# Kernel optimization log

Measured on AMD Instinct MI355X. Metric: run time of the kernel, lower is better.

The kernel has to match this reference:

```python
import jax, jax.numpy as jnp
import numpy as np
from jax import lax

CONV_SIZE = 5
MORPH_SIZE = 5
TH1_INIT = 0.5
STEP = 0.0005
LO, HI = 0.84, 0.86


def _maxpool(a):
    p = MORPH_SIZE // 2
    return lax.reduce_window(
        a, -jnp.inf, lax.max,
        window_dimensions=(1, 1, MORPH_SIZE, MORPH_SIZE),
        window_strides=(1, 1, 1, 1),
        padding=[(0, 0), (0, 0), (p, p), (p, p)])


def setup_inputs() -> dict:
    key = jax.random.key(0)
    k1, _ = jax.random.split(key)
    x = jax.random.uniform(k1, (8, 4, 1024, 1024), dtype=jnp.float32)
    blur_k = jnp.full((1, 1, CONV_SIZE, CONV_SIZE), 1.0 / CONV_SIZE ** 2, dtype=jnp.float32)
    return {"x": x, "blur_k": blur_k}


def reference(x, blur_k):
    N, c, h, w = x.shape
    xi = x.reshape(N * c, 1, h, w)
    out = lax.conv_general_dilated(
        xi, blur_k, window_strides=(1, 1), padding='SAME',
        dimension_numbers=('NCHW', 'OIHW', 'NCHW')).reshape(N, c, h, w)

    # iterative mean-based threshold (quantile) search, same as the torch while-loops
    out_c = lax.stop_gradient(out)

    def frac_above(th):
        return jnp.mean(jnp.where(out_c > th, 1.0, 0.0))

    th = jnp.float32(TH1_INIT)
    th = lax.while_loop(lambda t: frac_above(t) < LO, lambda t: t - STEP, th)
    th = lax.while_loop(lambda t: frac_above(t) > HI, lambda t: t + STEP, th)

    thr = jnp.where(out > th, 1.0, 0.0)
    # morphological close: max-pool then min-pool (min = -maxpool(-x))
    closed = -_maxpool(-_maxpool(thr))
    return closed  # torch casts to float64; kept float32 (see notes)
```

## Files before the change

### kernel.cpp

```cpp
#include <hip/hip_runtime.h>


#define K_STEPS 1024
#define LO_COUNT 28185723u
#define R_TILE 16
#define PT_ROWS 16

#define OFF_HIST 4096
#define OFF_KQ   16384

typedef float  fx4 __attribute__((ext_vector_type(4)));

struct TTable { float v[K_STEPS]; };
static constexpr TTable make_T() {
    TTable t{};
    float th = 0.5f;
    for (int k = 0; k < K_STEPS; k++) { t.v[k] = th; th = th - 0.0005f; }
    return t;
}
__device__ constexpr TTable Tc = make_T();

__device__ __forceinline__ uint4 cvt4(float4 f) {
    return make_uint4((unsigned int)(f.x * 8388608.0f),
                      (unsigned int)(f.y * 8388608.0f),
                      (unsigned int)(f.z * 8388608.0f),
                      (unsigned int)(f.w * 8388608.0f));
}

__device__ __forceinline__ int find_ki(const unsigned int* __restrict__ Us,
                                       float gbias, unsigned int s) {
    float g = fmaf(-(float)s, 9.5367432e-6f, gbias);
    int lo = (int)g;
    lo = max(0, min(1022, lo));
    unsigned int a0 = Us[lo], a1 = Us[lo + 1];
    return lo + (int)(s < a0) + (int)(s < a1);
}

__global__ __launch_bounds__(256, 8) void
k_pass1(const float4* __restrict__ x4, const float* __restrict__ bk,
        unsigned int* __restrict__ hist, unsigned short* __restrict__ kq16) {
    __shared__ unsigned int Us[K_STEPS];
    __shared__ unsigned int lh[K_STEPS + 1];
    int tid = threadIdx.x;
    int p = blockIdx.y, y0 = blockIdx.x * R_TILE;
    int wlane = tid & 63;

    {
        double c = (double)bk[0] * (1.0 / 8388608.0);
        #pragma unroll
        for (int i = 0; i < 4; i++) {
            int k = tid + 256 * i;
            double T = (double)Tc.v[k];
            unsigned int u = 0u;
            if (T >= 0.0) {
                u = (unsigned int)(floor(T / c) + 1.0);
                while (u > 0u && (double)(u - 1u) * c > T) u--;
                while (!((double)u * c > T)) u++;
            }
            Us[k] = u;
        }
    }
    for (int i = tid; i < K_STEPS + 1; i += 256) lh[i] = 0u;
    __syncthreads();
    float gbias = fmaf((float)Us[0], 9.5367432e-6f, 0.5f);

    const float4* pf = x4 + (size_t)p * 262144;
    int tB = (tid < 255) ? tid + 1 : 0;
    const uint4 z4 = make_uint4(0u, 0u, 0u, 0u);
    bool edge = (wlane == 63);

    unsigned int cs0 = 0, cs1 = 0, cs2 = 0, cs3 = 0;
    unsigned int cb0 = 0, cb1 = 0, cb2 = 0, cb3 = 0;
    {
        float4 ra[5], rb[5];
        #pragma unroll
        for (int i = 0; i < 5; i++) {
            int yy = y0 - 2 + i, yc = min(max(yy, 0), 1023);
            ra[i] = pf[yc * 256 + tid];
            if (edge) rb[i] = pf[yc * 256 + tB];
        }
        #pragma unroll
        for (int i = 0; i < 5; i++) {
            bool v = (unsigned)(y0 - 2 + i) < 1024u;
            uint4 a = v ? cvt4(ra[i]) : z4;
            cs0 += a.x; cs1 += a.y; cs2 += a.z; cs3 += a.w;
            if (edge) {
                uint4 b = v ? cvt4(rb[i]) : z4;
                cb0 += b.x; cb1 += b.y; cb2 += b.z; cb3 += b.w;
            }
        }
    }
    float4 N0a, N1a, O0a, O1a, NBa, OBa;
    {
        int yn0 = min(y0 + 3, 1023), yn1 = min(y0 + 4, 1023);
        int yo0 = max(y0 - 2, 0),    yo1 = max(y0 - 1, 0);
        N0a = pf[yn0 * 256 + tid]; N1a = pf[yn1 * 256 + tid];
        O0a = pf[yo0 * 256 + tid]; O1a = pf[yo1 * 256 + tid];
        if (edge) { NBa = pf[yn0 * 256 + tB]; OBa = pf[yo0 * 256 + tB]; }
    }

    unsigned int cnt0 = 0;
    #pragma unroll 4
    for (int iy = 0; iy < R_TILE; iy++) {
        int y = y0 + iy;

        unsigned int nc0 = __shfl_down(cs0, 1);
        unsigned int nc1 = __shfl_down(cs1, 1);
        unsigned int nc2 = __shfl_down(cs2, 1);
        unsigned int nc3 = __shfl_down(cs3, 1);
        if (edge) { nc0 = cb0; nc1 = cb1; nc2 = cb2; nc3 = cb3; }

        unsigned int m123 = cs1 + cs2 + cs3;
        unsigned int h45  = nc0 + nc1;
        unsigned int v0, v1, v2, v3;
        if (tid != 255) {
            v0 = cs0 + m123 + nc0;
            v1 = m123 + h45;
            v2 = cs2 + cs3 + h45 + nc2;
            v3 = cs3 + h45 + nc2 + nc3;
        } else {
            v0 = cs0 + m123;
            v1 = m123;
            v2 = h45 + nc2;
            v3 = h45 + nc2 + nc3;
        }

        int k0 = find_ki(Us, gbias, v0);
        int k1 = find_ki(Us, gbias, v1);
        int k2 = find_ki(Us, gbias, v2);
        int k3 = find_ki(Us, gbias, v3);
        cnt0 += (unsigned)(k0 == 0) + (unsigned)(k1 == 0)
              + (unsigned)(k2 == 0) + (unsigned)(k3 == 0);
        if (k0 > 0) atomicAdd(&lh[k0], 1u);
        if (k1 > 0) atomicAdd(&lh[k1], 1u);
        if (k2 > 0) atomicAdd(&lh[k2], 1u);
        if (k3 > 0) atomicAdd(&lh[k3], 1u);

        unsigned int pa = (unsigned)min(k0, 255) | ((unsigned)min(k1, 255) << 8);
        unsigned int pb = (unsigned)min(k2, 255) | ((unsigned)min(k3, 255) << 8);
        unsigned int paN = __shfl_down(pa, 1);
        size_t rb = ((size_t)p * 1024 + (size_t)y) * 512;
        if (wlane < 63) {
            ((unsigned int*)(kq16 + rb))[tid + 1] = pb | (paN << 16);
        } else {
            kq16[rb + ((tid < 255) ? (unsigned)(2 * tid + 2) : 0u)] =
                (unsigned short)pb;
        }
        if (wlane == 0) kq16[rb + 2 * tid + 1] = (unsigned short)pa;

        {
            bool vn = (unsigned)(y + 3) < 1024u;
            bool vo = (y - 2) >= 0;
            uint4 na = vn ? cvt4(N0a) : z4;
            uint4 oa = vo ? cvt4(O0a) : z4;
            cs0 += na.x - oa.x; cs1 += na.y - oa.y;
            cs2 += na.z - oa.z; cs3 += na.w - oa.w;
            if (edge) {
                uint4 nb = vn ? cvt4(NBa) : z4;
                uint4 ob = vo ? cvt4(OBa) : z4;
                cb0 += nb.x - ob.x; cb1 += nb.y - ob.y;
                cb2 += nb.z - ob.z; cb3 += nb.w - ob.w;
            }
        }
        N0a = N1a; O0a = O1a;
        {
            int yn = min(y + 5, 1023);
            N1a = pf[yn * 256 + tid];
            O1a = pf[y * 256 + tid];
            if (edge) {
                int ynb = min(y + 4, 1023), yob = max(y - 1, 0);
                NBa = pf[ynb * 256 + tB];
                OBa = pf[yob * 256 + tB];
            }
        }
    }

    #pragma unroll
    for (int d = 32; d > 0; d >>= 1) cnt0 += __shfl_down(cnt0, d);
    if ((tid & 63) == 0 && cnt0) atomicAdd(&lh[0], cnt0);
    __syncthreads();
    for (int i = tid; i < K_STEPS + 1; i += 256) {
        unsigned int c = lh[i];
        if (c) atomicAdd(&hist[i], c);
    }
}

__global__ __launch_bounds__(256) void
k_post(const unsigned char* __restrict__ kqb, const unsigned int* __restrict__ hist,
       float* __restrict__ out) {
    __shared__ unsigned long long Tt[24 * 16];
    __shared__ unsigned long long Vv[20 * 16];
    __shared__ unsigned long long Dd[20 * 16];
    __shared__ unsigned long long Ww[16 * 16];
    __shared__ unsigned long long Ff[16 * 16];
    __shared__ int ksS;

    int tid = threadIdx.x;
    int p = blockIdx.y, y0 = blockIdx.x * PT_ROWS;

    if (tid < 64) {
        int lane = tid;
        unsigned int h[16], s = 0;
        #pragma unroll
        for (int i = 0; i < 16; i++) { h[i] = hist[lane * 16 + i]; s += h[i]; }
        unsigned int inc = s;
        #pragma unroll
        for (int d = 1; d < 64; d <<= 1) {
            unsigned int t = __shfl_up(inc, d);
            if (lane >= d) inc += t;
        }
        unsigned int excl = inc - s;
        bool cross = (excl < LO_COUNT) && (excl + s >= LO_COUNT);
        unsigned long long m = __ballot(cross);
        if (m) {
            int cl = __ffsll((long long)m) - 1;
            if (lane == cl) {
                unsigned int c = excl; int ks = K_STEPS - 1;
                for (int i = 0; i < 16; i++) { c += h[i]; if (c >= LO_COUNT) { ks = lane * 16 + i; break; } }
                ksS = ks;
            }
        } else if (lane == 0) ksS = K_STEPS - 1;
    }
    __syncthreads();
    int ks = ksS;

    const unsigned char* kp = kqb + (size_t)p * 1048576;
    unsigned short* Tt16 = (unsigned short*)Tt;
    #pragma unroll
    for (int i = 0; i < 6; i++) {
        int ch = tid + 256 * i;
        int r = ch >> 6, cc = ch & 63;
        int pr = y0 - 4 + r;
        unsigned int m = 0u;
        if ((unsigned)pr < 1024u) {
            uint4 q = ((const uint4*)(kp + (size_t)pr * 1024))[cc];
            unsigned int wv;
            wv = q.x;
            m |= (unsigned)((wv & 0xffu) <= (unsigned)ks)
               | ((unsigned)(((wv >> 8) & 0xffu) <= (unsigned)ks) << 1)
               | ((unsigned)(((wv >> 16) & 0xffu) <= (unsigned)ks) << 2)
               | ((unsigned)((wv >> 24) <= (unsigned)ks) << 3);
            wv = q.y;
            m |= ((unsigned)((wv & 0xffu) <= (unsigned)ks) << 4)
               | ((unsigned)(((wv >> 8) & 0xffu) <= (unsigned)ks) << 5)
               | ((unsigned)(((wv >> 16) & 0xffu) <= (unsigned)ks) << 6)
               | ((unsigned)((wv >> 24) <= (unsigned)ks) << 7);
            wv = q.z;
            m |= ((unsigned)((wv & 0xffu) <= (unsigned)ks) << 8)
               | ((unsigned)(((wv >> 8) & 0xffu) <= (unsigned)ks) << 9)
               | ((unsigned)(((wv >> 16) & 0xffu) <= (unsigned)ks) << 10)
               | ((unsigned)((wv >> 24) <= (unsigned)ks) << 11);
            wv = q.w;
            m |= ((unsigned)((wv & 0xffu) <= (unsigned)ks) << 12)
               | ((unsigned)(((wv >> 8) & 0xffu) <= (unsigned)ks) << 13)
               | ((unsigned)(((wv >> 16) & 0xffu) <= (unsigned)ks) << 14)
               | ((unsigned)((wv >> 24) <= (unsigned)ks) << 15);
        }
        Tt16[ch] = (unsigned short)m;
    }
    __syncthreads();

    for (int i = tid; i < 320; i += 256) {
        int vr = i >> 4, wc = i & 15;
        int b = vr * 16 + wc;
        Vv[i] = Tt[b] | Tt[b + 16] | Tt[b + 32] | Tt[b + 48] | Tt[b + 64];
    }
    __syncthreads();

    for (int i = tid; i < 320; i += 256) {
        int vr = i >> 4, wc = i & 15;
        int pr = y0 - 2 + vr;
        if ((unsigned)pr >= 1024u) { Dd[i] = ~0ull; continue; }
        unsigned long long Vc = Vv[i];
        unsigned long long Vl = (wc > 0)  ? Vv[i - 1] : 0ull;
        unsigned long long Vr = (wc < 15) ? Vv[i + 1] : 0ull;
        Dd[i] = Vc
            | (Vc << 1) | (Vl >> 63)
            | (Vc << 2) | (Vl >> 62)
            | (Vc >> 1) | (Vr << 63)
            | (Vc >> 2) | (Vr << 62);
    }
    __syncthreads();

    {
        int wr = tid >> 4, wc = tid & 15;
        int b = wr * 16 + wc;
        Ww[tid] = Dd[b] & Dd[b + 16] & Dd[b + 32] & Dd[b + 48] & Dd[b + 64];
    }
    __syncthreads();

    {
        int wc = tid & 15;
        unsigned long long Wc = Ww[tid];
        unsigned long long Wl = (wc > 0)  ? Ww[tid - 1] : ~0ull;
        unsigned long long Wr = (wc < 15) ? Ww[tid + 1] : ~0ull;
        Ff[tid] = Wc
            & ((Wc << 1) | (Wl >> 63))
            & ((Wc << 2) | (Wl >> 62))
            & ((Wc >> 1) | (Wr << 63))
            & ((Wc >> 2) | (Wr << 62));
    }
    __syncthreads();

    for (int i = 0; i < PT_ROWS; i++) {
        unsigned long long wd = Ff[i * 16 + (tid >> 4)];
        int sh = (tid & 15) * 4;
        fx4 f;
        f.x = (float)((wd >> sh) & 1ull);
        f.y = (float)((wd >> (sh + 1)) & 1ull);
        f.z = (float)((wd >> (sh + 2)) & 1ull);
        f.w = (float)((wd >> (sh + 3)) & 1ull);
        fx4* dst = (fx4*)(out + (size_t)p * 1048576 + (size_t)(y0 + i) * 1024) + tid;
        __builtin_nontemporal_store(f, dst);
    }
}

extern "C" void kernel_launch(void* const* d_in, const int* in_sizes, int n_in,
                              void* d_out, int out_size, void* d_ws, size_t ws_size,
                              hipStream_t stream) {
    const float4* x4 = (const float4*)d_in[0];
    const float*  bk = (const float*)d_in[1];
    float* out = (float*)d_out;

    char* ws = (char*)d_ws;
    unsigned int*   hist = (unsigned int*)(ws + OFF_HIST);
    unsigned short* kq16 = (unsigned short*)(ws + OFF_KQ);
    const unsigned char* kqb = (const unsigned char*)(ws + OFF_KQ);

    (void)hipMemsetAsync(hist, 0, (K_STEPS + 1) * sizeof(unsigned int), stream);

    dim3 g1(1024 / R_TILE, 32);
    k_pass1<<<g1, 256, 0, stream>>>(x4, bk, hist, kq16);

    dim3 g2(1024 / PT_ROWS, 32);
    k_post<<<g2, 256, 0, stream>>>(kqb, hist, out);
}
```

Baseline: 292.8 us.

## Drop pass1 register prefetch pipeline and hoist post-kernel loads before histogram scan

```diff
diff --git a/kernel.cpp b/kernel.cpp
--- a/kernel.cpp
+++ b/kernel.cpp
@@ -36,7 +36,7 @@
     return lo + (int)(s < a0) + (int)(s < a1);
 }
 
-__global__ __launch_bounds__(256, 8) void
+__global__ __launch_bounds__(256, 6) void
 k_pass1(const float4* __restrict__ x4, const float* __restrict__ bk,
         unsigned int* __restrict__ hist, unsigned short* __restrict__ kq16) {
     __shared__ unsigned int Us[K_STEPS];
@@ -90,19 +90,17 @@
             }
         }
     }
-    float4 N0a, N1a, O0a, O1a, NBa, OBa;
-    {
-        int yn0 = min(y0 + 3, 1023), yn1 = min(y0 + 4, 1023);
-        int yo0 = max(y0 - 2, 0),    yo1 = max(y0 - 1, 0);
-        N0a = pf[yn0 * 256 + tid]; N1a = pf[yn1 * 256 + tid];
-        O0a = pf[yo0 * 256 + tid]; O1a = pf[yo1 * 256 + tid];
-        if (edge) { NBa = pf[yn0 * 256 + tB]; OBa = pf[yo0 * 256 + tB]; }
-    }
 
     unsigned int cnt0 = 0;
     #pragma unroll 4
     for (int iy = 0; iy < R_TILE; iy++) {
         int y = y0 + iy;
+
+        int yn = min(y + 3, 1023), yo = max(y - 2, 0);
+        float4 Na = pf[yn * 256 + tid];
+        float4 Oa = pf[yo * 256 + tid];
+        float4 Nb, Ob;
+        if (edge) { Nb = pf[yn * 256 + tB]; Ob = pf[yo * 256 + tB]; }
 
         unsigned int nc0 = __shfl_down(cs0, 1);
         unsigned int nc1 = __shfl_down(cs1, 1);
@@ -151,28 +149,17 @@
         {
             bool vn = (unsigned)(y + 3) < 1024u;
             bool vo = (y - 2) >= 0;
-            uint4 na = vn ? cvt4(N0a) : z4;
-            uint4 oa = vo ? cvt4(O0a) : z4;
+            uint4 na = vn ? cvt4(Na) : z4;
+            uint4 oa = vo ? cvt4(Oa) : z4;
             cs0 += na.x - oa.x; cs1 += na.y - oa.y;
             cs2 += na.z - oa.z; cs3 += na.w - oa.w;
             if (edge) {
-                uint4 nb = vn ? cvt4(NBa) : z4;
-                uint4 ob = vo ? cvt4(OBa) : z4;
+                uint4 nb = vn ? cvt4(Nb) : z4;
+                uint4 ob = vo ? cvt4(Ob) : z4;
                 cb0 += nb.x - ob.x; cb1 += nb.y - ob.y;
                 cb2 += nb.z - ob.z; cb3 += nb.w - ob.w;
             }
         }
-        N0a = N1a; O0a = O1a;
-        {
-            int yn = min(y + 5, 1023);
-            N1a = pf[yn * 256 + tid];
-            O1a = pf[y * 256 + tid];
-            if (edge) {
-                int ynb = min(y + 4, 1023), yob = max(y - 1, 0);
-                NBa = pf[ynb * 256 + tB];
-                OBa = pf[yob * 256 + tB];
-            }
-        }
     }
 
     #pragma unroll
@@ -185,7 +172,7 @@
     }
 }
 
-__global__ __launch_bounds__(256) void
+__global__ __launch_bounds__(256, 6) void
 k_post(const unsigned char* __restrict__ kqb, const unsigned int* __restrict__ hist,
        float* __restrict__ out) {
     __shared__ unsigned long long Tt[24 * 16];
@@ -197,6 +184,24 @@
 
     int tid = threadIdx.x;
     int p = blockIdx.y, y0 = blockIdx.x * PT_ROWS;
+
+    const unsigned char* kp = kqb + (size_t)p * 1048576;
+    uint4 q0, q1, q2, q3, q4, q5;
+    {
+        const uint4 zq = make_uint4(0u, 0u, 0u, 0u);
+        #pragma unroll
+        for (int i = 0; i < 6; i++) {
+            int ch = tid + 256 * i;
+            int r = ch >> 6, cc = ch & 63;
+            int pr = y0 - 4 + r;
+            uint4 q = zq;
+            if ((unsigned)pr < 1024u)
+                q = ((const uint4*)(kp + (size_t)pr * 1024))[cc];
+            if (i == 0) q0 = q; else if (i == 1) q1 = q;
+            else if (i == 2) q2 = q; else if (i == 3) q3 = q;
+            else if (i == 4) q4 = q; else q5 = q;
+        }
+    }
 
     if (tid < 64) {
         int lane = tid;
@@ -224,38 +229,37 @@
     __syncthreads();
     int ks = ksS;
 
-    const unsigned char* kp = kqb + (size_t)p * 1048576;
     unsigned short* Tt16 = (unsigned short*)Tt;
     #pragma unroll
     for (int i = 0; i < 6; i++) {
+        uint4 q = (i == 0) ? q0 : (i == 1) ? q1 : (i == 2) ? q2
+                : (i == 3) ? q3 : (i == 4) ? q4 : q5;
         int ch = tid + 256 * i;
-        int r = ch >> 6, cc = ch & 63;
+        int r = ch >> 6;
         int pr = y0 - 4 + r;
         unsigned int m = 0u;
-        if ((unsigned)pr < 1024u) {
-            uint4 q = ((const uint4*)(kp + (size_t)pr * 1024))[cc];
-            unsigned int wv;
-            wv = q.x;
-            m |= (unsigned)((wv & 0xffu) <= (unsigned)ks)
-               | ((unsigned)(((wv >> 8) & 0xffu) <= (unsigned)ks) << 1)
-               | ((unsigned)(((wv >> 16) & 0xffu) <= (unsigned)ks) << 2)
-               | ((unsigned)((wv >> 24) <= (unsigned)ks) << 3);
-            wv = q.y;
-            m |= ((unsigned)((wv & 0xffu) <= (unsigned)ks) << 4)
-               | ((unsigned)(((wv >> 8) & 0xffu) <= (unsigned)ks) << 5)
-               | ((unsigned)(((wv >> 16) & 0xffu) <= (unsigned)ks) << 6)
-               | ((unsigned)((wv >> 24) <= (unsigned)ks) << 7);
-            wv = q.z;
-            m |= ((unsigned)((wv & 0xffu) <= (unsigned)ks) << 8)
-               | ((unsigned)(((wv >> 8) & 0xffu) <= (unsigned)ks) << 9)
-               | ((unsigned)(((wv >> 16) & 0xffu) <= (unsigned)ks) << 10)
-               | ((unsigned)((wv >> 24) <= (unsigned)ks) << 11);
-            wv = q.w;
-            m |= ((unsigned)((wv & 0xffu) <= (unsigned)ks) << 12)
-               | ((unsigned)(((wv >> 8) & 0xffu) <= (unsigned)ks) << 13)
-               | ((unsigned)(((wv >> 16) & 0xffu) <= (unsigned)ks) << 14)
-               | ((unsigned)((wv >> 24) <= (unsigned)ks) << 15);
-        }
+        unsigned int wv;
+        wv = q.x;
+        m |= (unsigned)((wv & 0xffu) <= (unsigned)ks)
+           | ((unsigned)(((wv >> 8) & 0xffu) <= (unsigned)ks) << 1)
+           | ((unsigned)(((wv >> 16) & 0xffu) <= (unsigned)ks) << 2)
+           | ((unsigned)((wv >> 24) <= (unsigned)ks) << 3);
+        wv = q.y;
+        m |= ((unsigned)((wv & 0xffu) <= (unsigned)ks) << 4)
+           | ((unsigned)(((wv >> 8) & 0xffu) <= (unsigned)ks) << 5)
+           | ((unsigned)(((wv >> 16) & 0xffu) <= (unsigned)ks) << 6)
+           | ((unsigned)((wv >> 24) <= (unsigned)ks) << 7);
+        wv = q.z;
+        m |= ((unsigned)((wv & 0xffu) <= (unsigned)ks) << 8)
+           | ((unsigned)(((wv >> 8) & 0xffu) <= (unsigned)ks) << 9)
+           | ((unsigned)(((wv >> 16) & 0xffu) <= (unsigned)ks) << 10)
+           | ((unsigned)((wv >> 24) <= (unsigned)ks) << 11);
+        wv = q.w;
+        m |= ((unsigned)((wv & 0xffu) <= (unsigned)ks) << 12)
+           | ((unsigned)(((wv >> 8) & 0xffu) <= (unsigned)ks) << 13)
+           | ((unsigned)(((wv >> 16) & 0xffu) <= (unsigned)ks) << 14)
+           | ((unsigned)((wv >> 24) <= (unsigned)ks) << 15);
+        if ((unsigned)pr >= 1024u) m = 0u;
         Tt16[ch] = (unsigned short)m;
     }
     __syncthreads();
```

Result: no change. 289.1 us (-1.3%).
